# Kernel tuning notes

Measured on AMD Instinct MI355X. Metric: run time of the kernel, lower is better.

## Reference

```python
import jax, jax.numpy as jnp
import numpy as np

T, H, E, K = 256, 2048, 60, 4          # tokens, hidden, num_experts, top_k
F, FS = 1408, 5632                      # moe_intermediate, shared_expert_intermediate


def setup_inputs() -> dict:
    key = jax.random.key(0)
    ks = jax.random.split(key, 9)
    s = 0.02  # weight init scale to keep activations sane
    return {
        "hidden_states": jax.random.normal(ks[0], (T, H), jnp.float32),
        "gate_w": jax.random.normal(ks[1], (H, E), jnp.float32) * s,       # router
        "w_gate": jax.random.normal(ks[2], (E, H, F), jnp.float32) * s,    # expert gate proj
        "w_up": jax.random.normal(ks[3], (E, H, F), jnp.float32) * s,      # expert up proj
        "w_down": jax.random.normal(ks[4], (E, F, H), jnp.float32) * s,    # expert down proj
        "sw_gate": jax.random.normal(ks[5], (H, FS), jnp.float32) * s,     # shared expert gate proj
        "sw_up": jax.random.normal(ks[6], (H, FS), jnp.float32) * s,       # shared expert up proj
        "sw_down": jax.random.normal(ks[7], (FS, H), jnp.float32) * s,     # shared expert down proj
        "shared_gate_w": jax.random.normal(ks[8], (H, 1), jnp.float32) * s,  # shared expert sigmoid gate
    }


def reference(hidden_states, gate_w, w_gate, w_up, w_down, sw_gate, sw_up, sw_down, shared_gate_w):
    x = hidden_states                                  # [T, H]
    # --- router: softmax then top-k (DefaultMoeRoutingMethod, no renorm) ---
    probs = jax.nn.softmax(x @ gate_w, axis=-1)        # [T, E]
    vals, idx = jax.lax.top_k(probs, K)                # [T, K]
    tok = jnp.arange(x.shape[0])[:, None]
    comb = jnp.zeros_like(probs).at[tok, idx].set(vals)  # dense combine weights [T, E]
    # --- experts: gated SiLU MLP per expert, combine-weighted (down is linear,
    #     so scaling the pre-down activation by comb equals scaling the output) ---
    g = jnp.einsum('th,ehf->tef', x, w_gate)           # [T, E, F]
    u = jnp.einsum('th,ehf->tef', x, w_up)             # [T, E, F]
    a = (jax.nn.silu(g) * u) * comb[:, :, None]
    moe_out = jnp.einsum('tef,efh->th', a, w_down)     # [T, H]
    # --- shared expert with sigmoid gate ---
    sh = (jax.nn.silu(x @ sw_gate) * (x @ sw_up)) @ sw_down   # [T, H]
    sh = jax.nn.sigmoid(x @ shared_gate_w) * sh
    return moe_out + sh
```

## Files before the change

### kernel.cpp

```cpp
#include <hip/hip_runtime.h>
#include <hip/hip_bf16.h>
#include <stdint.h>

typedef unsigned short ushort_t;
typedef uint32_t u32;
typedef __attribute__((ext_vector_type(8))) __bf16 bf16x8;
typedef __attribute__((ext_vector_type(8))) unsigned short u16x8;
typedef __attribute__((ext_vector_type(4))) float f32x4;

#define T_  256
#define H_  2048
#define E_  60
#define F_  1408
#define FS_ 5632

__device__ __forceinline__ u32 rne2(float lo, float hi){
  u32 a = __builtin_bit_cast(u32, lo);
  u32 b = __builtin_bit_cast(u32, hi);
  a += 0x7FFFu + ((a >> 16) & 1u);
  b += 0x7FFFu + ((b >> 16) & 1u);
  return (a >> 16) | (b & 0xFFFF0000u);
}
__device__ __forceinline__ ushort_t rne1(float f){
  u32 a = __builtin_bit_cast(u32, f);
  a += 0x7FFFu + ((a >> 16) & 1u);
  return (ushort_t)(a >> 16);
}
__device__ __forceinline__ f32x4 zero4(){ f32x4 z; z[0]=0.f; z[1]=0.f; z[2]=0.f; z[3]=0.f; return z; }

__device__ __forceinline__ bf16x8 ldsbS(const float* p, const int S){
  union { u32 u[4]; bf16x8 v; } cv;
  cv.u[0] = rne2(p[0],   p[S]);
  cv.u[1] = rne2(p[2*S], p[3*S]);
  cv.u[2] = rne2(p[4*S], p[5*S]);
  cv.u[3] = rne2(p[6*S], p[7*S]);
  return cv.v;
}
__device__ __forceinline__ bf16x8 loada(const ushort_t* p){
  return __builtin_bit_cast(bf16x8, *(const u16x8*)p);
}
__device__ __forceinline__ void gload16(const float* g, float* l){
  __builtin_amdgcn_global_load_lds(
      (const __attribute__((address_space(1))) void*)g,
      (__attribute__((address_space(3))) void*)l, 16, 0, 0);
}
#define MFMA(a,b,c) __builtin_amdgcn_mfma_f32_16x16x32_bf16((a),(b),(c),0,0,0)

#define VMW(n)  asm volatile("s_waitcnt vmcnt(" #n ")" ::: "memory")
#define BARM()  asm volatile("s_barrier" ::: "memory")
#define SCH()   __builtin_amdgcn_sched_barrier(0)

__global__ __launch_bounds__(256) void k_router(
    const float* __restrict__ x, const float* __restrict__ gw,
    const float* __restrict__ sgw, ushort_t* __restrict__ xb,
    int* __restrict__ tk_idx, float* __restrict__ tk_val, float* __restrict__ sig)
{
  const int t = blockIdx.x, tid = threadIdx.x;
  const float* xr = x + (size_t)t * H_;
  {
    const float4 v0 = *(const float4*)(xr + tid*8);
    const float4 v1 = *(const float4*)(xr + tid*8 + 4);
    u32* dst = (u32*)(xb + (size_t)t*H_ + tid*8);
    dst[0] = rne2(v0.x, v0.y); dst[1] = rne2(v0.z, v0.w);
    dst[2] = rne2(v1.x, v1.y); dst[3] = rne2(v1.z, v1.w);
  }
  __shared__ float s_part[4][64];
  __shared__ float s_logit[64];
  __shared__ float s_red[256];
  const int e = tid & 63, q = tid >> 6;
  float p = 0.f;
  if (e < E_) {
    const float* g = gw + e;
    for (int h = q*512; h < q*512 + 512; ++h) p += xr[h] * g[h*E_];
  }
  s_part[q][e] = p;
  float sp = 0.f;
  for (int h = tid; h < H_; h += 256) sp += xr[h] * sgw[h];
  s_red[tid] = sp;
  __syncthreads();
  if (tid < 64) s_logit[tid] = s_part[0][tid] + s_part[1][tid] + s_part[2][tid] + s_part[3][tid];
  for (int s = 128; s > 0; s >>= 1) {
    if (tid < s) s_red[tid] += s_red[tid + s];
    __syncthreads();
  }
  if (tid == 0) {
    sig[t] = 1.f / (1.f + expf(-s_red[0]));
    float mx = -3.4e38f;
    for (int i = 0; i < E_; ++i) mx = fmaxf(mx, s_logit[i]);
    float sum = 0.f;
    for (int i = 0; i < E_; ++i) sum += expf(s_logit[i] - mx);
    for (int k = 0; k < 4; ++k) {
      float bv = -3.4e38f; int bi = 0;
      for (int i = 0; i < E_; ++i) { float v = s_logit[i]; if (v > bv) { bv = v; bi = i; } }
      tk_idx[t*4 + k] = bi;
      tk_val[t*4 + k] = expf(bv - mx) / sum;
      s_logit[bi] = -3.4e38f;
    }
  }
}

__global__ void k_lists(const int* __restrict__ tk_idx, const float* __restrict__ tk_val,
                        int* __restrict__ cnt, int* __restrict__ ltok,
                        int* __restrict__ lpair, float* __restrict__ lwt)
{
  const int e = threadIdx.x;
  if (e >= E_) return;
  int c = 0;
  for (int t = 0; t < T_; ++t) {
    #pragma unroll
    for (int k = 0; k < 4; ++k) {
      int ei = tk_idx[t*4 + k];
      if (ei == e && c < 64) {
        ltok[e*64 + c] = t;
        lpair[e*64 + c] = t*4 + k;
        lwt[e*64 + c] = tk_val[t*4 + k];
        ++c;
      }
    }
  }
  cnt[e] = c;
}

__global__ __launch_bounds__(256) void k_moe_gu(
    const ushort_t* __restrict__ xb, const float* __restrict__ wg_all,
    const float* __restrict__ wu_all, const int* __restrict__ cnt,
    const int* __restrict__ ltok, const float* __restrict__ lwt,
    ushort_t* __restrict__ act)
{
  __shared__ float lds[2][2*32*128];
  const int e = blockIdx.y;
  int m = cnt[e];
  if (m == 0) return;
  if (m > 64) m = 64;
  const int tid = threadIdx.x, wave = tid >> 6, lane = tid & 63;
  const int ln15 = lane & 15, kg = lane >> 4;
  const int col0 = blockIdx.x * 128;
  const size_t wbase = (size_t)e * ((size_t)H_ * F_) + col0;
  const float* gsg = wg_all + wbase + (size_t)(lane >> 5) * F_ + (lane & 31) * 4;
  const float* gsu = wu_all + wbase + (size_t)(lane >> 5) * F_ + (lane & 31) * 4;
  const int r0 = wave * 8;

  const ushort_t* ap[4];
  #pragma unroll
  for (int rt = 0; rt < 4; ++rt) {
    int row = rt*16 + ln15;
    int tok = ltok[e*64 + (row < m ? row : m-1)];
    ap[rt] = xb + (size_t)tok * H_ + kg*8;
  }

  f32x4 ag[4][2], au[4][2];
  #pragma unroll
  for (int i = 0; i < 4; ++i) { ag[i][0]=zero4(); ag[i][1]=zero4(); au[i][0]=zero4(); au[i][1]=zero4(); }
  bf16x8 a0[4], a1[4];

#define GU_STAGE(B, K0) do { \
    _Pragma("unroll") for (int i2 = 0; i2 < 4; ++i2) { \
      int r_ = r0 + i2*2; \
      gload16(gsg + (size_t)(K0 + r_) * F_, &lds[B][r_*128]); \
      gload16(gsu + (size_t)(K0 + r_) * F_, &lds[B][4096 + r_*128]); \
    } } while(0)
#define GU_ALOAD(D, K0) do { \
    _Pragma("unroll") for (int rt = 0; rt < 4; ++rt) D[rt] = loada(ap[rt] + (K0)); } while(0)
#define GU_COMPUTE(B, A) do { \
    const float* lg_ = &lds[B][kg*1024 + wave*32 + ln15]; \
    bf16x8 bg0_ = ldsbS(lg_, 128), bg1_ = ldsbS(lg_ + 16, 128); \
    bf16x8 bu0_ = ldsbS(lg_ + 4096, 128), bu1_ = ldsbS(lg_ + 4112, 128); \
    _Pragma("unroll") for (int rt = 0; rt < 4; ++rt) { \
      ag[rt][0] = MFMA(A[rt], bg0_, ag[rt][0]); \
      ag[rt][1] = MFMA(A[rt], bg1_, ag[rt][1]); \
      au[rt][0] = MFMA(A[rt], bu0_, au[rt][0]); \
      au[rt][1] = MFMA(A[rt], bu1_, au[rt][1]); \
    } } while(0)

  GU_ALOAD(a0, 0);  GU_STAGE(0, 0);
  GU_ALOAD(a1, 32); GU_STAGE(1, 32);
  for (int t = 0; t + 2 < 64; t += 2) {
    VMW(12); BARM(); SCH();
    GU_COMPUTE(0, a0);
    BARM();
    GU_ALOAD(a0, (t+2)*32); GU_STAGE(0, (t+2)*32);
    VMW(12); BARM(); SCH();
    GU_COMPUTE(1, a1);
    BARM();
    GU_ALOAD(a1, (t+3)*32); GU_STAGE(1, (t+3)*32);
  }
  VMW(12); BARM(); SCH();
  GU_COMPUTE(0, a0);
  VMW(0); BARM(); SCH();
  GU_COMPUTE(1, a1);

  #pragma unroll
  for (int rt = 0; rt < 4; ++rt)
    #pragma unroll
    for (int nt = 0; nt < 2; ++nt)
      #pragma unroll
      for (int j = 0; j < 4; ++j) {
        int r = rt*16 + kg*4 + j;
        if (r < m) {
          float wt = lwt[e*64 + r];
          float g = ag[rt][nt][j], u = au[rt][nt][j];
          float a = g / (1.f + __expf(-g)) * u * wt;
          act[((size_t)e*64 + r) * F_ + col0 + wave*32 + nt*16 + ln15] = rne1(a);
        }
      }
}

__global__ __launch_bounds__(256) void k_moe_down(
    const ushort_t* __restrict__ act, const float* __restrict__ wd_all,
    const int* __restrict__ cnt, const int* __restrict__ lpair,
    float* __restrict__ out4)
{
  __shared__ float lds[2][32*128];
  __shared__ int s_pair[64];
  const int e = blockIdx.y;
  int m = cnt[e];
  if (m == 0) return;
  if (m > 64) m = 64;
  const int tid = threadIdx.x, wave = tid >> 6, lane = tid & 63;
  const int ln15 = lane & 15, kg = lane >> 4;
  if (tid < 64) s_pair[tid] = (tid < m) ? lpair[e*64 + tid] : 0;
  const int col0 = blockIdx.x * 128;
  const float* gsd = wd_all + (size_t)e * ((size_t)F_ * H_) + col0
                   + (size_t)(lane >> 5) * H_ + (lane & 31) * 4;
  const int r0 = wave * 8;

  const ushort_t* ap[4];
  #pragma unroll
  for (int rt = 0; rt < 4; ++rt)
    ap[rt] = act + ((size_t)e*64 + rt*16 + ln15) * F_ + kg*8;

  f32x4 ac[4][2];
  #pragma unroll
  for (int i = 0; i < 4; ++i) { ac[i][0]=zero4(); ac[i][1]=zero4(); }
  bf16x8 a0[4], a1[4];

#define DN_STAGE(B, K0) do { \
    _Pragma("unroll") for (int i2 = 0; i2 < 4; ++i2) { \
      int r_ = r0 + i2*2; \
      gload16(gsd + (size_t)(K0 + r_) * H_, &lds[B][r_*128]); \
    } } while(0)
#define DN_ALOAD(D, K0) do { \
    _Pragma("unroll") for (int rt = 0; rt < 4; ++rt) D[rt] = loada(ap[rt] + (K0)); } while(0)
#define DN_COMPUTE(B, A) do { \
    const float* lw_ = &lds[B][kg*1024 + wave*32 + ln15]; \
    bf16x8 b0_ = ldsbS(lw_, 128), b1_ = ldsbS(lw_ + 16, 128); \
    _Pragma("unroll") for (int rt = 0; rt < 4; ++rt) { \
      ac[rt][0] = MFMA(A[rt], b0_, ac[rt][0]); \
      ac[rt][1] = MFMA(A[rt], b1_, ac[rt][1]); \
    } } while(0)

  DN_ALOAD(a0, 0);  DN_STAGE(0, 0);
  DN_ALOAD(a1, 32); DN_STAGE(1, 32);
  for (int t = 0; t + 2 < 44; t += 2) {
    VMW(8); BARM(); SCH();
    DN_COMPUTE(0, a0);
    BARM();
    DN_ALOAD(a0, (t+2)*32); DN_STAGE(0, (t+2)*32);
    VMW(8); BARM(); SCH();
    DN_COMPUTE(1, a1);
    BARM();
    DN_ALOAD(a1, (t+3)*32); DN_STAGE(1, (t+3)*32);
  }
  VMW(8); BARM(); SCH();
  DN_COMPUTE(0, a0);
  VMW(0); BARM(); SCH();
  DN_COMPUTE(1, a1);

  #pragma unroll
  for (int rt = 0; rt < 4; ++rt)
    #pragma unroll
    for (int nt = 0; nt < 2; ++nt)
      #pragma unroll
      for (int j = 0; j < 4; ++j) {
        int r = rt*16 + kg*4 + j;
        if (r < m)
          out4[(size_t)s_pair[r] * H_ + col0 + wave*32 + nt*16 + ln15] = ac[rt][nt][j];
      }
}

__global__ __launch_bounds__(256) void k_sh_gu(
    const ushort_t* __restrict__ xb, const float* __restrict__ swg,
    const float* __restrict__ swu, ushort_t* __restrict__ acts)
{
  __shared__ float lds[2][2048];
  const int tid = threadIdx.x, wave = tid >> 6, lane = tid & 63;
  const int ln15 = lane & 15, kg = lane >> 4;
  const int cb = blockIdx.x * 32;
  const int rowb = wave * 64;
  const int r0 = wave * 8;
  const float* gsg = swg + (size_t)(lane >> 3) * FS_ + cb + (lane & 7) * 4;
  const float* gsu = swu + (size_t)(lane >> 3) * FS_ + cb + (lane & 7) * 4;

  const ushort_t* ap[4];
  #pragma unroll
  for (int rt = 0; rt < 4; ++rt)
    ap[rt] = xb + (size_t)(rowb + rt*16 + ln15) * H_ + kg*8;

  f32x4 ag[4][2], au[4][2];
  #pragma unroll
  for (int i = 0; i < 4; ++i) { ag[i][0]=zero4(); ag[i][1]=zero4(); au[i][0]=zero4(); au[i][1]=zero4(); }
  bf16x8 a0[4], a1[4];

#define SG_STAGE(B, K0) do { \
    gload16(gsg + (size_t)(K0 + r0) * FS_, &lds[B][r0*32]); \
    gload16(gsu + (size_t)(K0 + r0) * FS_, &lds[B][1024 + r0*32]); \
  } while(0)
#define SG_ALOAD(D, K0) do { \
    _Pragma("unroll") for (int rt = 0; rt < 4; ++rt) D[rt] = loada(ap[rt] + (K0)); } while(0)
#define SG_COMPUTE(B, A) do { \
    const float* lg_ = &lds[B][kg*256 + ln15]; \
    bf16x8 bg0_ = ldsbS(lg_, 32), bg1_ = ldsbS(lg_ + 16, 32); \
    bf16x8 bu0_ = ldsbS(lg_ + 1024, 32), bu1_ = ldsbS(lg_ + 1040, 32); \
    _Pragma("unroll") for (int rt = 0; rt < 4; ++rt) { \
      ag[rt][0] = MFMA(A[rt], bg0_, ag[rt][0]); \
      ag[rt][1] = MFMA(A[rt], bg1_, ag[rt][1]); \
      au[rt][0] = MFMA(A[rt], bu0_, au[rt][0]); \
      au[rt][1] = MFMA(A[rt], bu1_, au[rt][1]); \
    } } while(0)

  SG_ALOAD(a0, 0);  SG_STAGE(0, 0);
  SG_ALOAD(a1, 32); SG_STAGE(1, 32);
  for (int t = 0; t + 2 < 64; t += 2) {
    VMW(6); BARM(); SCH();
    SG_COMPUTE(0, a0);
    BARM();
    SG_ALOAD(a0, (t+2)*32); SG_STAGE(0, (t+2)*32);
    VMW(6); BARM(); SCH();
    SG_COMPUTE(1, a1);
    BARM();
    SG_ALOAD(a1, (t+3)*32); SG_STAGE(1, (t+3)*32);
  }
  VMW(6); BARM(); SCH();
  SG_COMPUTE(0, a0);
  VMW(0); BARM(); SCH();
  SG_COMPUTE(1, a1);

  #pragma unroll
  for (int rt = 0; rt < 4; ++rt)
    #pragma unroll
    for (int nt = 0; nt < 2; ++nt)
      #pragma unroll
      for (int j = 0; j < 4; ++j) {
        int row = rowb + rt*16 + kg*4 + j;
        float g = ag[rt][nt][j], u = au[rt][nt][j];
        acts[(size_t)row * FS_ + cb + nt*16 + ln15] = rne1(g / (1.f + __expf(-g)) * u);
      }
}

__global__ __launch_bounds__(256) void k_sh_down(
    const ushort_t* __restrict__ acts, const float* __restrict__ swd,
    float* __restrict__ acc4)
{
  __shared__ float lds[2][2048];
  const int tid = threadIdx.x, wave = tid >> 6, lane = tid & 63;
  const int ln15 = lane & 15, kg = lane >> 4;
  const int cb = blockIdx.x * 64;
  const int kh = blockIdx.y;
  const int rowb = wave * 64;
  const int r0 = wave * 8;
  const float* gsd = swd + (size_t)(kh*1408) * H_ + cb
                   + (size_t)(lane >> 4) * H_ + (lane & 15) * 4;

  const ushort_t* ap[4];
  #pragma unroll
  for (int rt = 0; rt < 4; ++rt)
    ap[rt] = acts + (size_t)(rowb + rt*16 + ln15) * FS_ + kh*1408 + kg*8;

  f32x4 ac[4][4];
  #pragma unroll
  for (int i = 0; i < 4; ++i)
    #pragma unroll
    for (int c = 0; c < 4; ++c) ac[i][c] = zero4();
  bf16x8 a0[4], a1[4];

#define SD_STAGE(B, K0) do { \
    gload16(gsd + (size_t)(K0 + r0) * H_,     &lds[B][r0*64]); \
    gload16(gsd + (size_t)(K0 + r0 + 4) * H_, &lds[B][(r0+4)*64]); \
  } while(0)
#define SD_ALOAD(D, K0) do { \
    _Pragma("unroll") for (int rt = 0; rt < 4; ++rt) D[rt] = loada(ap[rt] + (K0)); } while(0)
#define SD_COMPUTE(B, A) do { \
    const float* lw_ = &lds[B][kg*512 + ln15]; \
    bf16x8 b0_ = ldsbS(lw_, 64),      b1_ = ldsbS(lw_ + 16, 64); \
    bf16x8 b2_ = ldsbS(lw_ + 32, 64), b3_ = ldsbS(lw_ + 48, 64); \
    _Pragma("unroll") for (int rt = 0; rt < 4; ++rt) { \
      ac[rt][0] = MFMA(A[rt], b0_, ac[rt][0]); \
      ac[rt][1] = MFMA(A[rt], b1_, ac[rt][1]); \
      ac[rt][2] = MFMA(A[rt], b2_, ac[rt][2]); \
      ac[rt][3] = MFMA(A[rt], b3_, ac[rt][3]); \
    } } while(0)

  SD_ALOAD(a0, 0);  SD_STAGE(0, 0);
  SD_ALOAD(a1, 32); SD_STAGE(1, 32);
  for (int t = 0; t + 2 < 44; t += 2) {
    VMW(6); BARM(); SCH();
    SD_COMPUTE(0, a0);
    BARM();
    SD_ALOAD(a0, (t+2)*32); SD_STAGE(0, (t+2)*32);
    VMW(6); BARM(); SCH();
    SD_COMPUTE(1, a1);
    BARM();
    SD_ALOAD(a1, (t+3)*32); SD_STAGE(1, (t+3)*32);
  }
  VMW(6); BARM(); SCH();
  SD_COMPUTE(0, a0);
  VMW(0); BARM(); SCH();
  SD_COMPUTE(1, a1);

  #pragma unroll
  for (int rt = 0; rt < 4; ++rt)
    #pragma unroll
    for (int c = 0; c < 4; ++c)
      #pragma unroll
      for (int j = 0; j < 4; ++j) {
        int row = rowb + rt*16 + kg*4 + j;
        acc4[((size_t)kh * T_ + row) * H_ + cb + c*16 + ln15] = ac[rt][c][j];
      }
}

__global__ __launch_bounds__(256) void k_final(
    const float* __restrict__ acc4, const float* __restrict__ out4,
    const float* __restrict__ sig, float* __restrict__ out)
{
  const int idx = blockIdx.x * blockDim.x + threadIdx.x;
  const int t = idx >> 9;
  const int h = (idx & 511) * 4;
  float ox = 0.f, oy = 0.f, oz = 0.f, ow = 0.f;
  #pragma unroll
  for (int s = 0; s < 4; ++s) {
    const float4 v = *(const float4*)(acc4 + ((size_t)s * T_ + t) * H_ + h);
    ox += v.x; oy += v.y; oz += v.z; ow += v.w;
  }
  const float sg = sig[t];
  ox *= sg; oy *= sg; oz *= sg; ow *= sg;
  #pragma unroll
  for (int k = 0; k < 4; ++k) {
    const float4 e4 = *(const float4*)(out4 + (size_t)(t*4 + k) * H_ + h);
    ox += e4.x; oy += e4.y; oz += e4.z; ow += e4.w;
  }
  float4 o; o.x = ox; o.y = oy; o.z = oz; o.w = ow;
  *(float4*)(out + (size_t)t * H_ + h) = o;
}

extern "C" void kernel_launch(void* const* d_in, const int* in_sizes, int n_in,
                              void* d_out, int out_size, void* d_ws, size_t ws_size,
                              hipStream_t stream)
{
  (void)in_sizes; (void)n_in; (void)out_size; (void)ws_size;
  const float* x   = (const float*)d_in[0];
  const float* gw  = (const float*)d_in[1];
  const float* wg  = (const float*)d_in[2];
  const float* wu  = (const float*)d_in[3];
  const float* wd  = (const float*)d_in[4];
  const float* swg = (const float*)d_in[5];
  const float* swu = (const float*)d_in[6];
  const float* swd = (const float*)d_in[7];
  const float* sgw = (const float*)d_in[8];

  char* ws = (char*)d_ws;
  ushort_t* xb    = (ushort_t*)(ws);
  ushort_t* act   = (ushort_t*)(ws + 1048576);
  ushort_t* acts  = (ushort_t*)(ws + 11862016);
  float*    out4  = (float*)   (ws + 14745600);
  float*    acc4  = (float*)   (ws + 23134208);
  float*    sig   = (float*)   (ws + 31522816);
  int*      tkidx = (int*)     (ws + 31523840);
  float*    tkval = (float*)   (ws + 31527936);
  int*      cnt   = (int*)     (ws + 31532032);
  int*      ltok  = (int*)     (ws + 31532288);
  int*      lpair = (int*)     (ws + 31547648);
  float*    lwt   = (float*)   (ws + 31563008);

  k_router  <<<T_, 256, 0, stream>>>(x, gw, sgw, xb, tkidx, tkval, sig);
  k_lists   <<<1, 64, 0, stream>>>(tkidx, tkval, cnt, ltok, lpair, lwt);
  k_moe_gu  <<<dim3(F_/128, E_), 256, 0, stream>>>(xb, wg, wu, cnt, ltok, lwt, act);
  k_moe_down<<<dim3(H_/128, E_), 256, 0, stream>>>(act, wd, cnt, lpair, out4);
  k_sh_gu   <<<dim3(FS_/32), 256, 0, stream>>>(xb, swg, swu, acts);
  k_sh_down <<<dim3(H_/64, 4), 256, 0, stream>>>(acts, swd, acc4);
  k_final   <<<512, 256, 0, stream>>>(acc4, out4, sig, (float*)d_out);
}
```

Baseline: 671.8 us.

## Halve MoE expert column tile to 64 and stage routing lists through LDS

The expert gate/up and down kernels now use 64-column tiles instead of 128, doubling the grid along the column axis. This gives more blocks for the weight-streaming, memory-bound expert GEMMs across the GPU's CUs, at the cost of more redundant activation loads and fewer MFMAs per LDS fetch. The list-building kernel also loads the top-k indices and values into shared memory with 256 threads before each expert scans them, replacing repeated global reads.

```diff
diff --git a/kernel.cpp b/kernel.cpp
--- a/kernel.cpp
+++ b/kernel.cpp
@@ -99,23 +99,25 @@
   }
 }
 
-__global__ void k_lists(const int* __restrict__ tk_idx, const float* __restrict__ tk_val,
-                        int* __restrict__ cnt, int* __restrict__ ltok,
-                        int* __restrict__ lpair, float* __restrict__ lwt)
-{
-  const int e = threadIdx.x;
+__global__ __launch_bounds__(256) void k_lists(
+    const int* __restrict__ tk_idx, const float* __restrict__ tk_val,
+    int* __restrict__ cnt, int* __restrict__ ltok,
+    int* __restrict__ lpair, float* __restrict__ lwt)
+{
+  __shared__ int   s_idx[1024];
+  __shared__ float s_val[1024];
+  const int tid = threadIdx.x;
+  for (int i = tid; i < 1024; i += 256) { s_idx[i] = tk_idx[i]; s_val[i] = tk_val[i]; }
+  __syncthreads();
+  const int e = tid;
   if (e >= E_) return;
   int c = 0;
-  for (int t = 0; t < T_; ++t) {
-    #pragma unroll
-    for (int k = 0; k < 4; ++k) {
-      int ei = tk_idx[t*4 + k];
-      if (ei == e && c < 64) {
-        ltok[e*64 + c] = t;
-        lpair[e*64 + c] = t*4 + k;
-        lwt[e*64 + c] = tk_val[t*4 + k];
-        ++c;
-      }
+  for (int i = 0; i < 1024; ++i) {
+    if (s_idx[i] == e && c < 64) {
+      ltok[e*64 + c]  = i >> 2;
+      lpair[e*64 + c] = i;
+      lwt[e*64 + c]   = s_val[i];
+      ++c;
     }
   }
   cnt[e] = c;
@@ -127,17 +129,17 @@
     const int* __restrict__ ltok, const float* __restrict__ lwt,
     ushort_t* __restrict__ act)
 {
-  __shared__ float lds[2][2*32*128];
+  __shared__ float lds[2][2*32*64];
   const int e = blockIdx.y;
   int m = cnt[e];
   if (m == 0) return;
   if (m > 64) m = 64;
   const int tid = threadIdx.x, wave = tid >> 6, lane = tid & 63;
   const int ln15 = lane & 15, kg = lane >> 4;
-  const int col0 = blockIdx.x * 128;
+  const int col0 = blockIdx.x * 64;
   const size_t wbase = (size_t)e * ((size_t)H_ * F_) + col0;
-  const float* gsg = wg_all + wbase + (size_t)(lane >> 5) * F_ + (lane & 31) * 4;
-  const float* gsu = wu_all + wbase + (size_t)(lane >> 5) * F_ + (lane & 31) * 4;
+  const float* gsg = wg_all + wbase + (size_t)(lane >> 4) * F_ + (lane & 15) * 4;
+  const float* gsu = wu_all + wbase + (size_t)(lane >> 4) * F_ + (lane & 15) * 4;
   const int r0 = wave * 8;
 
   const ushort_t* ap[4];
@@ -148,43 +150,41 @@
     ap[rt] = xb + (size_t)tok * H_ + kg*8;
   }
 
-  f32x4 ag[4][2], au[4][2];
-  #pragma unroll
-  for (int i = 0; i < 4; ++i) { ag[i][0]=zero4(); ag[i][1]=zero4(); au[i][0]=zero4(); au[i][1]=zero4(); }
+  f32x4 ag[4], au[4];
+  #pragma unroll
+  for (int i = 0; i < 4; ++i) { ag[i] = zero4(); au[i] = zero4(); }
   bf16x8 a0[4], a1[4];
 
 #define GU_STAGE(B, K0) do { \
-    _Pragma("unroll") for (int i2 = 0; i2 < 4; ++i2) { \
-      int r_ = r0 + i2*2; \
-      gload16(gsg + (size_t)(K0 + r_) * F_, &lds[B][r_*128]); \
-      gload16(gsu + (size_t)(K0 + r_) * F_, &lds[B][4096 + r_*128]); \
-    } } while(0)
+    gload16(gsg + (size_t)(K0 + r0)     * F_, &lds[B][r0*64]); \
+    gload16(gsg + (size_t)(K0 + r0 + 4) * F_, &lds[B][(r0+4)*64]); \
+    gload16(gsu + (size_t)(K0 + r0)     * F_, &lds[B][2048 + r0*64]); \
+    gload16(gsu + (size_t)(K0 + r0 + 4) * F_, &lds[B][2048 + (r0+4)*64]); \
+  } while(0)
 #define GU_ALOAD(D, K0) do { \
     _Pragma("unroll") for (int rt = 0; rt < 4; ++rt) D[rt] = loada(ap[rt] + (K0)); } while(0)
 #define GU_COMPUTE(B, A) do { \
-    const float* lg_ = &lds[B][kg*1024 + wave*32 + ln15]; \
-    bf16x8 bg0_ = ldsbS(lg_, 128), bg1_ = ldsbS(lg_ + 16, 128); \
-    bf16x8 bu0_ = ldsbS(lg_ + 4096, 128), bu1_ = ldsbS(lg_ + 4112, 128); \
+    const float* lg_ = &lds[B][kg*512 + wave*16 + ln15]; \
+    bf16x8 bg_ = ldsbS(lg_, 64); \
+    bf16x8 bu_ = ldsbS(lg_ + 2048, 64); \
     _Pragma("unroll") for (int rt = 0; rt < 4; ++rt) { \
-      ag[rt][0] = MFMA(A[rt], bg0_, ag[rt][0]); \
-      ag[rt][1] = MFMA(A[rt], bg1_, ag[rt][1]); \
-      au[rt][0] = MFMA(A[rt], bu0_, au[rt][0]); \
-      au[rt][1] = MFMA(A[rt], bu1_, au[rt][1]); \
+      ag[rt] = MFMA(A[rt], bg_, ag[rt]); \
+      au[rt] = MFMA(A[rt], bu_, au[rt]); \
     } } while(0)
 
   GU_ALOAD(a0, 0);  GU_STAGE(0, 0);
   GU_ALOAD(a1, 32); GU_STAGE(1, 32);
   for (int t = 0; t + 2 < 64; t += 2) {
-    VMW(12); BARM(); SCH();
+    VMW(8); BARM(); SCH();
     GU_COMPUTE(0, a0);
     BARM();
     GU_ALOAD(a0, (t+2)*32); GU_STAGE(0, (t+2)*32);
-    VMW(12); BARM(); SCH();
+    VMW(8); BARM(); SCH();
     GU_COMPUTE(1, a1);
     BARM();
     GU_ALOAD(a1, (t+3)*32); GU_STAGE(1, (t+3)*32);
   }
-  VMW(12); BARM(); SCH();
+  VMW(8); BARM(); SCH();
   GU_COMPUTE(0, a0);
   VMW(0); BARM(); SCH();
   GU_COMPUTE(1, a1);
@@ -192,17 +192,15 @@
   #pragma unroll
   for (int rt = 0; rt < 4; ++rt)
     #pragma unroll
-    for (int nt = 0; nt < 2; ++nt)
-      #pragma unroll
-      for (int j = 0; j < 4; ++j) {
-        int r = rt*16 + kg*4 + j;
-        if (r < m) {
-          float wt = lwt[e*64 + r];
-          float g = ag[rt][nt][j], u = au[rt][nt][j];
-          float a = g / (1.f + __expf(-g)) * u * wt;
-          act[((size_t)e*64 + r) * F_ + col0 + wave*32 + nt*16 + ln15] = rne1(a);
-        }
+    for (int j = 0; j < 4; ++j) {
+      int r = rt*16 + kg*4 + j;
+      if (r < m) {
+        float wt = lwt[e*64 + r];
+        float g = ag[rt][j], u = au[rt][j];
+        float a = g / (1.f + __expf(-g)) * u * wt;
+        act[((size_t)e*64 + r) * F_ + col0 + wave*16 + ln15] = rne1(a);
       }
+    }
 }
 
 __global__ __launch_bounds__(256) void k_moe_down(
@@ -210,7 +208,7 @@
     const int* __restrict__ cnt, const int* __restrict__ lpair,
     float* __restrict__ out4)
 {
-  __shared__ float lds[2][32*128];
+  __shared__ float lds[2][32*64];
   __shared__ int s_pair[64];
   const int e = blockIdx.y;
   int m = cnt[e];
@@ -219,9 +217,9 @@
   const int tid = threadIdx.x, wave = tid >> 6, lane = tid & 63;
   const int ln15 = lane & 15, kg = lane >> 4;
   if (tid < 64) s_pair[tid] = (tid < m) ? lpair[e*64 + tid] : 0;
-  const int col0 = blockIdx.x * 128;
+  const int col0 = blockIdx.x * 64;
   const float* gsd = wd_all + (size_t)e * ((size_t)F_ * H_) + col0
-                   + (size_t)(lane >> 5) * H_ + (lane & 31) * 4;
+                   + (size_t)(lane >> 4) * H_ + (lane & 15) * 4;
   const int r0 = wave * 8;
 
   const ushort_t* ap[4];
@@ -229,39 +227,37 @@
   for (int rt = 0; rt < 4; ++rt)
     ap[rt] = act + ((size_t)e*64 + rt*16 + ln15) * F_ + kg*8;
 
-  f32x4 ac[4][2];
-  #pragma unroll
-  for (int i = 0; i < 4; ++i) { ac[i][0]=zero4(); ac[i][1]=zero4(); }
+  f32x4 ac[4];
+  #pragma unroll
+  for (int i = 0; i < 4; ++i) ac[i] = zero4();
   bf16x8 a0[4], a1[4];
 
 #define DN_STAGE(B, K0) do { \
-    _Pragma("unroll") for (int i2 = 0; i2 < 4; ++i2) { \
-      int r_ = r0 + i2*2; \
-      gload16(gsd + (size_t)(K0 + r_) * H_, &lds[B][r_*128]); \
-    } } while(0)
+    gload16(gsd + (size_t)(K0 + r0)     * H_, &lds[B][r0*64]); \
+    gload16(gsd + (size_t)(K0 + r0 + 4) * H_, &lds[B][(r0+4)*64]); \
+  } while(0)
 #define DN_ALOAD(D, K0) do { \
     _Pragma("unroll") for (int rt = 0; rt < 4; ++rt) D[rt] = loada(ap[rt] + (K0)); } while(0)
 #define DN_COMPUTE(B, A) do { \
-    const float* lw_ = &lds[B][kg*1024 + wave*32 + ln15]; \
-    bf16x8 b0_ = ldsbS(lw_, 128), b1_ = ldsbS(lw_ + 16, 128); \
-    _Pragma("unroll") for (int rt = 0; rt < 4; ++rt) { \
-      ac[rt][0] = MFMA(A[rt], b0_, ac[rt][0]); \
-      ac[rt][1] = MFMA(A[rt], b1_, ac[rt][1]); \
-    } } while(0)
+    const float* lw_ = &lds[B][kg*512 + wave*16 + ln15]; \
+    bf16x8 b_ = ldsbS(lw_, 64); \
+    _Pragma("unroll") for (int rt = 0; rt < 4; ++rt) \
+      ac[rt] = MFMA(A[rt], b_, ac[rt]); \
+  } while(0)
 
   DN_ALOAD(a0, 0);  DN_STAGE(0, 0);
   DN_ALOAD(a1, 32); DN_STAGE(1, 32);
   for (int t = 0; t + 2 < 44; t += 2) {
-    VMW(8); BARM(); SCH();
+    VMW(6); BARM(); SCH();
     DN_COMPUTE(0, a0);
     BARM();
     DN_ALOAD(a0, (t+2)*32); DN_STAGE(0, (t+2)*32);
-    VMW(8); BARM(); SCH();
+    VMW(6); BARM(); SCH();
     DN_COMPUTE(1, a1);
     BARM();
     DN_ALOAD(a1, (t+3)*32); DN_STAGE(1, (t+3)*32);
   }
-  VMW(8); BARM(); SCH();
+  VMW(6); BARM(); SCH();
   DN_COMPUTE(0, a0);
   VMW(0); BARM(); SCH();
   DN_COMPUTE(1, a1);
@@ -269,13 +265,11 @@
   #pragma unroll
   for (int rt = 0; rt < 4; ++rt)
     #pragma unroll
-    for (int nt = 0; nt < 2; ++nt)
-      #pragma unroll
-      for (int j = 0; j < 4; ++j) {
-        int r = rt*16 + kg*4 + j;
-        if (r < m)
-          out4[(size_t)s_pair[r] * H_ + col0 + wave*32 + nt*16 + ln15] = ac[rt][nt][j];
-      }
+    for (int j = 0; j < 4; ++j) {
+      int r = rt*16 + kg*4 + j;
+      if (r < m)
+        out4[(size_t)s_pair[r] * H_ + col0 + wave*16 + ln15] = ac[rt][j];
+    }
 }
 
 __global__ __launch_bounds__(256) void k_sh_gu(
@@ -472,9 +466,9 @@
   float*    lwt   = (float*)   (ws + 31563008);
 
   k_router  <<<T_, 256, 0, stream>>>(x, gw, sgw, xb, tkidx, tkval, sig);
-  k_lists   <<<1, 64, 0, stream>>>(tkidx, tkval, cnt, ltok, lpair, lwt);
-  k_moe_gu  <<<dim3(F_/128, E_), 256, 0, stream>>>(xb, wg, wu, cnt, ltok, lwt, act);
-  k_moe_down<<<dim3(H_/128, E_), 256, 0, stream>>>(act, wd, cnt, lpair, out4);
+  k_lists   <<<1, 256, 0, stream>>>(tkidx, tkval, cnt, ltok, lpair, lwt);
+  k_moe_gu  <<<dim3(F_/64, E_), 256, 0, stream>>>(xb, wg, wu, cnt, ltok, lwt, act);
+  k_moe_down<<<dim3(H_/64, E_), 256, 0, stream>>>(act, wd, cnt, lpair, out4);
   k_sh_gu   <<<dim3(FS_/32), 256, 0, stream>>>(xb, swg, swu, acts);
   k_sh_down <<<dim3(H_/64, 4), 256, 0, stream>>>(acts, swd, acc4);
   k_final   <<<512, 256, 0, stream>>>(acc4, out4, sig, (float*)d_out);
```

Result: slower. 716.3 us (+6.6%).

## Merge routed and shared expert GEMMs into two combined launches; widen down-proj tiles

Applied to the files above, without the earlier changes.

Combines the routed-expert gate/up kernel with the shared-expert gate/up kernel in one launch, and the routed down with the shared down in a second launch, with blocks picking their role by block index. The goal is to fill the GPU with independent work at once and to cut the tail effects of launching separate kernels back to back. The routed down projection now uses 256-column tiles, so each block reuses the activation tile across more columns. The list-building kernel stages top-k data in LDS and uses a flat scan. Each merged kernel reserves a fixed 64KB of LDS, which may reduce how many blocks fit on a CU.

```diff
diff --git a/kernel.cpp b/kernel.cpp
--- a/kernel.cpp
+++ b/kernel.cpp
@@ -99,70 +99,79 @@
   }
 }
 
-__global__ void k_lists(const int* __restrict__ tk_idx, const float* __restrict__ tk_val,
-                        int* __restrict__ cnt, int* __restrict__ ltok,
-                        int* __restrict__ lpair, float* __restrict__ lwt)
-{
-  const int e = threadIdx.x;
+__global__ __launch_bounds__(256) void k_lists(
+    const int* __restrict__ tk_idx, const float* __restrict__ tk_val,
+    int* __restrict__ cnt, int* __restrict__ ltok,
+    int* __restrict__ lpair, float* __restrict__ lwt)
+{
+  __shared__ int   s_idx[1024];
+  __shared__ float s_val[1024];
+  const int tid = threadIdx.x;
+  for (int i = tid; i < 1024; i += 256) { s_idx[i] = tk_idx[i]; s_val[i] = tk_val[i]; }
+  __syncthreads();
+  const int e = tid;
   if (e >= E_) return;
   int c = 0;
-  for (int t = 0; t < T_; ++t) {
-    #pragma unroll
-    for (int k = 0; k < 4; ++k) {
-      int ei = tk_idx[t*4 + k];
-      if (ei == e && c < 64) {
-        ltok[e*64 + c] = t;
-        lpair[e*64 + c] = t*4 + k;
-        lwt[e*64 + c] = tk_val[t*4 + k];
-        ++c;
-      }
+  for (int i = 0; i < 1024; ++i) {
+    if (s_idx[i] == e && c < 64) {
+      ltok[e*64 + c]  = i >> 2;
+      lpair[e*64 + c] = i;
+      lwt[e*64 + c]   = s_val[i];
+      ++c;
     }
   }
   cnt[e] = c;
 }
 
-__global__ __launch_bounds__(256) void k_moe_gu(
-    const ushort_t* __restrict__ xb, const float* __restrict__ wg_all,
-    const float* __restrict__ wu_all, const int* __restrict__ cnt,
-    const int* __restrict__ ltok, const float* __restrict__ lwt,
-    ushort_t* __restrict__ act)
-{
-  __shared__ float lds[2][2*32*128];
-  const int e = blockIdx.y;
-  int m = cnt[e];
-  if (m == 0) return;
-  if (m > 64) m = 64;
+__global__ __launch_bounds__(256) void k_mega1(
+    const ushort_t* __restrict__ xb,
+    const float* __restrict__ wg_all, const float* __restrict__ wu_all,
+    const int* __restrict__ cnt, const int* __restrict__ ltok,
+    const float* __restrict__ lwt, ushort_t* __restrict__ act,
+    const float* __restrict__ swg, const float* __restrict__ swu,
+    ushort_t* __restrict__ acts)
+{
+  __shared__ char smem[65536];
+  float* lds = (float*)smem;
+  const int bid = blockIdx.x;
   const int tid = threadIdx.x, wave = tid >> 6, lane = tid & 63;
   const int ln15 = lane & 15, kg = lane >> 4;
-  const int col0 = blockIdx.x * 128;
-  const size_t wbase = (size_t)e * ((size_t)H_ * F_) + col0;
-  const float* gsg = wg_all + wbase + (size_t)(lane >> 5) * F_ + (lane & 31) * 4;
-  const float* gsu = wu_all + wbase + (size_t)(lane >> 5) * F_ + (lane & 31) * 4;
-  const int r0 = wave * 8;
-
-  const ushort_t* ap[4];
-  #pragma unroll
-  for (int rt = 0; rt < 4; ++rt) {
-    int row = rt*16 + ln15;
-    int tok = ltok[e*64 + (row < m ? row : m-1)];
-    ap[rt] = xb + (size_t)tok * H_ + kg*8;
-  }
-
-  f32x4 ag[4][2], au[4][2];
-  #pragma unroll
-  for (int i = 0; i < 4; ++i) { ag[i][0]=zero4(); ag[i][1]=zero4(); au[i][0]=zero4(); au[i][1]=zero4(); }
-  bf16x8 a0[4], a1[4];
+
+  if (bid < 660) {
+    const int e  = bid / 11;
+    const int cx = bid % 11;
+    int m = cnt[e];
+    if (m == 0) return;
+    if (m > 64) m = 64;
+    const int col0 = cx * 128;
+    const size_t wbase = (size_t)e * ((size_t)H_ * F_) + col0;
+    const float* gsg = wg_all + wbase + (size_t)(lane >> 5) * F_ + (lane & 31) * 4;
+    const float* gsu = wu_all + wbase + (size_t)(lane >> 5) * F_ + (lane & 31) * 4;
+    const int r0 = wave * 8;
+
+    const ushort_t* ap[4];
+    #pragma unroll
+    for (int rt = 0; rt < 4; ++rt) {
+      int row = rt*16 + ln15;
+      int tok = ltok[e*64 + (row < m ? row : m-1)];
+      ap[rt] = xb + (size_t)tok * H_ + kg*8;
+    }
+
+    f32x4 ag[4][2], au[4][2];
+    #pragma unroll
+    for (int i = 0; i < 4; ++i) { ag[i][0]=zero4(); ag[i][1]=zero4(); au[i][0]=zero4(); au[i][1]=zero4(); }
+    bf16x8 a0[4], a1[4];
 
 #define GU_STAGE(B, K0) do { \
     _Pragma("unroll") for (int i2 = 0; i2 < 4; ++i2) { \
       int r_ = r0 + i2*2; \
-      gload16(gsg + (size_t)(K0 + r_) * F_, &lds[B][r_*128]); \
-      gload16(gsu + (size_t)(K0 + r_) * F_, &lds[B][4096 + r_*128]); \
+      gload16(gsg + (size_t)(K0 + r_) * F_, lds + (B)*8192 + r_*128); \
+      gload16(gsu + (size_t)(K0 + r_) * F_, lds + (B)*8192 + 4096 + r_*128); \
     } } while(0)
 #define GU_ALOAD(D, K0) do { \
     _Pragma("unroll") for (int rt = 0; rt < 4; ++rt) D[rt] = loada(ap[rt] + (K0)); } while(0)
 #define GU_COMPUTE(B, A) do { \
-    const float* lg_ = &lds[B][kg*1024 + wave*32 + ln15]; \
+    const float* lg_ = lds + (B)*8192 + kg*1024 + wave*32 + ln15; \
     bf16x8 bg0_ = ldsbS(lg_, 128), bg1_ = ldsbS(lg_ + 16, 128); \
     bf16x8 bu0_ = ldsbS(lg_ + 4096, 128), bu1_ = ldsbS(lg_ + 4112, 128); \
     _Pragma("unroll") for (int rt = 0; rt < 4; ++rt) { \
@@ -172,143 +181,63 @@
       au[rt][1] = MFMA(A[rt], bu1_, au[rt][1]); \
     } } while(0)
 
-  GU_ALOAD(a0, 0);  GU_STAGE(0, 0);
-  GU_ALOAD(a1, 32); GU_STAGE(1, 32);
-  for (int t = 0; t + 2 < 64; t += 2) {
+    GU_ALOAD(a0, 0);  GU_STAGE(0, 0);
+    GU_ALOAD(a1, 32); GU_STAGE(1, 32);
+    for (int t = 0; t + 2 < 64; t += 2) {
+      VMW(12); BARM(); SCH();
+      GU_COMPUTE(0, a0);
+      BARM();
+      GU_ALOAD(a0, (t+2)*32); GU_STAGE(0, (t+2)*32);
+      VMW(12); BARM(); SCH();
+      GU_COMPUTE(1, a1);
+      BARM();
+      GU_ALOAD(a1, (t+3)*32); GU_STAGE(1, (t+3)*32);
+    }
     VMW(12); BARM(); SCH();
     GU_COMPUTE(0, a0);
-    BARM();
-    GU_ALOAD(a0, (t+2)*32); GU_STAGE(0, (t+2)*32);
-    VMW(12); BARM(); SCH();
+    VMW(0); BARM(); SCH();
     GU_COMPUTE(1, a1);
-    BARM();
-    GU_ALOAD(a1, (t+3)*32); GU_STAGE(1, (t+3)*32);
-  }
-  VMW(12); BARM(); SCH();
-  GU_COMPUTE(0, a0);
-  VMW(0); BARM(); SCH();
-  GU_COMPUTE(1, a1);
-
-  #pragma unroll
-  for (int rt = 0; rt < 4; ++rt)
-    #pragma unroll
-    for (int nt = 0; nt < 2; ++nt)
-      #pragma unroll
-      for (int j = 0; j < 4; ++j) {
-        int r = rt*16 + kg*4 + j;
-        if (r < m) {
-          float wt = lwt[e*64 + r];
-          float g = ag[rt][nt][j], u = au[rt][nt][j];
-          float a = g / (1.f + __expf(-g)) * u * wt;
-          act[((size_t)e*64 + r) * F_ + col0 + wave*32 + nt*16 + ln15] = rne1(a);
+
+    #pragma unroll
+    for (int rt = 0; rt < 4; ++rt)
+      #pragma unroll
+      for (int nt = 0; nt < 2; ++nt)
+        #pragma unroll
+        for (int j = 0; j < 4; ++j) {
+          int r = rt*16 + kg*4 + j;
+          if (r < m) {
+            float wt = lwt[e*64 + r];
+            float g = ag[rt][nt][j], u = au[rt][nt][j];
+            float a = g / (1.f + __expf(-g)) * u * wt;
+            act[((size_t)e*64 + r) * F_ + col0 + wave*32 + nt*16 + ln15] = rne1(a);
+          }
         }
-      }
-}
-
-__global__ __launch_bounds__(256) void k_moe_down(
-    const ushort_t* __restrict__ act, const float* __restrict__ wd_all,
-    const int* __restrict__ cnt, const int* __restrict__ lpair,
-    float* __restrict__ out4)
-{
-  __shared__ float lds[2][32*128];
-  __shared__ int s_pair[64];
-  const int e = blockIdx.y;
-  int m = cnt[e];
-  if (m == 0) return;
-  if (m > 64) m = 64;
-  const int tid = threadIdx.x, wave = tid >> 6, lane = tid & 63;
-  const int ln15 = lane & 15, kg = lane >> 4;
-  if (tid < 64) s_pair[tid] = (tid < m) ? lpair[e*64 + tid] : 0;
-  const int col0 = blockIdx.x * 128;
-  const float* gsd = wd_all + (size_t)e * ((size_t)F_ * H_) + col0
-                   + (size_t)(lane >> 5) * H_ + (lane & 31) * 4;
-  const int r0 = wave * 8;
-
-  const ushort_t* ap[4];
-  #pragma unroll
-  for (int rt = 0; rt < 4; ++rt)
-    ap[rt] = act + ((size_t)e*64 + rt*16 + ln15) * F_ + kg*8;
-
-  f32x4 ac[4][2];
-  #pragma unroll
-  for (int i = 0; i < 4; ++i) { ac[i][0]=zero4(); ac[i][1]=zero4(); }
-  bf16x8 a0[4], a1[4];
-
-#define DN_STAGE(B, K0) do { \
-    _Pragma("unroll") for (int i2 = 0; i2 < 4; ++i2) { \
-      int r_ = r0 + i2*2; \
-      gload16(gsd + (size_t)(K0 + r_) * H_, &lds[B][r_*128]); \
-    } } while(0)
-#define DN_ALOAD(D, K0) do { \
-    _Pragma("unroll") for (int rt = 0; rt < 4; ++rt) D[rt] = loada(ap[rt] + (K0)); } while(0)
-#define DN_COMPUTE(B, A) do { \
-    const float* lw_ = &lds[B][kg*1024 + wave*32 + ln15]; \
-    bf16x8 b0_ = ldsbS(lw_, 128), b1_ = ldsbS(lw_ + 16, 128); \
-    _Pragma("unroll") for (int rt = 0; rt < 4; ++rt) { \
-      ac[rt][0] = MFMA(A[rt], b0_, ac[rt][0]); \
-      ac[rt][1] = MFMA(A[rt], b1_, ac[rt][1]); \
-    } } while(0)
-
-  DN_ALOAD(a0, 0);  DN_STAGE(0, 0);
-  DN_ALOAD(a1, 32); DN_STAGE(1, 32);
-  for (int t = 0; t + 2 < 44; t += 2) {
-    VMW(8); BARM(); SCH();
-    DN_COMPUTE(0, a0);
-    BARM();
-    DN_ALOAD(a0, (t+2)*32); DN_STAGE(0, (t+2)*32);
-    VMW(8); BARM(); SCH();
-    DN_COMPUTE(1, a1);
-    BARM();
-    DN_ALOAD(a1, (t+3)*32); DN_STAGE(1, (t+3)*32);
-  }
-  VMW(8); BARM(); SCH();
-  DN_COMPUTE(0, a0);
-  VMW(0); BARM(); SCH();
-  DN_COMPUTE(1, a1);
-
-  #pragma unroll
-  for (int rt = 0; rt < 4; ++rt)
-    #pragma unroll
-    for (int nt = 0; nt < 2; ++nt)
-      #pragma unroll
-      for (int j = 0; j < 4; ++j) {
-        int r = rt*16 + kg*4 + j;
-        if (r < m)
-          out4[(size_t)s_pair[r] * H_ + col0 + wave*32 + nt*16 + ln15] = ac[rt][nt][j];
-      }
-}
-
-__global__ __launch_bounds__(256) void k_sh_gu(
-    const ushort_t* __restrict__ xb, const float* __restrict__ swg,
-    const float* __restrict__ swu, ushort_t* __restrict__ acts)
-{
-  __shared__ float lds[2][2048];
-  const int tid = threadIdx.x, wave = tid >> 6, lane = tid & 63;
-  const int ln15 = lane & 15, kg = lane >> 4;
-  const int cb = blockIdx.x * 32;
-  const int rowb = wave * 64;
-  const int r0 = wave * 8;
-  const float* gsg = swg + (size_t)(lane >> 3) * FS_ + cb + (lane & 7) * 4;
-  const float* gsu = swu + (size_t)(lane >> 3) * FS_ + cb + (lane & 7) * 4;
-
-  const ushort_t* ap[4];
-  #pragma unroll
-  for (int rt = 0; rt < 4; ++rt)
-    ap[rt] = xb + (size_t)(rowb + rt*16 + ln15) * H_ + kg*8;
-
-  f32x4 ag[4][2], au[4][2];
-  #pragma unroll
-  for (int i = 0; i < 4; ++i) { ag[i][0]=zero4(); ag[i][1]=zero4(); au[i][0]=zero4(); au[i][1]=zero4(); }
-  bf16x8 a0[4], a1[4];
+  } else {
+    const int sb = bid - 660;
+    const int cb = sb * 32;
+    const int rowb = wave * 64;
+    const int r0 = wave * 8;
+    const float* gsg = swg + (size_t)(lane >> 3) * FS_ + cb + (lane & 7) * 4;
+    const float* gsu = swu + (size_t)(lane >> 3) * FS_ + cb + (lane & 7) * 4;
+
+    const ushort_t* ap[4];
+    #pragma unroll
+    for (int rt = 0; rt < 4; ++rt)
+      ap[rt] = xb + (size_t)(rowb + rt*16 + ln15) * H_ + kg*8;
+
+    f32x4 ag[4][2], au[4][2];
+    #pragma unroll
+    for (int i = 0; i < 4; ++i) { ag[i][0]=zero4(); ag[i][1]=zero4(); au[i][0]=zero4(); au[i][1]=zero4(); }
+    bf16x8 a0[4], a1[4];
 
 #define SG_STAGE(B, K0) do { \
-    gload16(gsg + (size_t)(K0 + r0) * FS_, &lds[B][r0*32]); \
-    gload16(gsu + (size_t)(K0 + r0) * FS_, &lds[B][1024 + r0*32]); \
+    gload16(gsg + (size_t)(K0 + r0) * FS_, lds + (B)*2048 + r0*32); \
+    gload16(gsu + (size_t)(K0 + r0) * FS_, lds + (B)*2048 + 1024 + r0*32); \
   } while(0)
 #define SG_ALOAD(D, K0) do { \
     _Pragma("unroll") for (int rt = 0; rt < 4; ++rt) D[rt] = loada(ap[rt] + (K0)); } while(0)
 #define SG_COMPUTE(B, A) do { \
-    const float* lg_ = &lds[B][kg*256 + ln15]; \
+    const float* lg_ = lds + (B)*2048 + kg*256 + ln15; \
     bf16x8 bg0_ = ldsbS(lg_, 32), bg1_ = ldsbS(lg_ + 16, 32); \
     bf16x8 bu0_ = ldsbS(lg_ + 1024, 32), bu1_ = ldsbS(lg_ + 1040, 32); \
     _Pragma("unroll") for (int rt = 0; rt < 4; ++rt) { \
@@ -318,69 +247,148 @@
       au[rt][1] = MFMA(A[rt], bu1_, au[rt][1]); \
     } } while(0)
 
-  SG_ALOAD(a0, 0);  SG_STAGE(0, 0);
-  SG_ALOAD(a1, 32); SG_STAGE(1, 32);
-  for (int t = 0; t + 2 < 64; t += 2) {
+    SG_ALOAD(a0, 0);  SG_STAGE(0, 0);
+    SG_ALOAD(a1, 32); SG_STAGE(1, 32);
+    for (int t = 0; t + 2 < 64; t += 2) {
+      VMW(6); BARM(); SCH();
+      SG_COMPUTE(0, a0);
+      BARM();
+      SG_ALOAD(a0, (t+2)*32); SG_STAGE(0, (t+2)*32);
+      VMW(6); BARM(); SCH();
+      SG_COMPUTE(1, a1);
+      BARM();
+      SG_ALOAD(a1, (t+3)*32); SG_STAGE(1, (t+3)*32);
+    }
     VMW(6); BARM(); SCH();
     SG_COMPUTE(0, a0);
-    BARM();
-    SG_ALOAD(a0, (t+2)*32); SG_STAGE(0, (t+2)*32);
-    VMW(6); BARM(); SCH();
+    VMW(0); BARM(); SCH();
     SG_COMPUTE(1, a1);
-    BARM();
-    SG_ALOAD(a1, (t+3)*32); SG_STAGE(1, (t+3)*32);
-  }
-  VMW(6); BARM(); SCH();
-  SG_COMPUTE(0, a0);
-  VMW(0); BARM(); SCH();
-  SG_COMPUTE(1, a1);
-
-  #pragma unroll
-  for (int rt = 0; rt < 4; ++rt)
-    #pragma unroll
-    for (int nt = 0; nt < 2; ++nt)
-      #pragma unroll
-      for (int j = 0; j < 4; ++j) {
-        int row = rowb + rt*16 + kg*4 + j;
-        float g = ag[rt][nt][j], u = au[rt][nt][j];
-        acts[(size_t)row * FS_ + cb + nt*16 + ln15] = rne1(g / (1.f + __expf(-g)) * u);
-      }
-}
-
-__global__ __launch_bounds__(256) void k_sh_down(
+
+    #pragma unroll
+    for (int rt = 0; rt < 4; ++rt)
+      #pragma unroll
+      for (int nt = 0; nt < 2; ++nt)
+        #pragma unroll
+        for (int j = 0; j < 4; ++j) {
+          int row = rowb + rt*16 + kg*4 + j;
+          float g = ag[rt][nt][j], u = au[rt][nt][j];
+          acts[(size_t)row * FS_ + cb + nt*16 + ln15] = rne1(g / (1.f + __expf(-g)) * u);
+        }
+  }
+}
+
+__global__ __launch_bounds__(256) void k_mega2(
+    const ushort_t* __restrict__ act, const float* __restrict__ wd_all,
+    const int* __restrict__ cnt, const int* __restrict__ lpair,
+    float* __restrict__ out4,
     const ushort_t* __restrict__ acts, const float* __restrict__ swd,
     float* __restrict__ acc4)
 {
-  __shared__ float lds[2][2048];
+  __shared__ char smem[65536];
+  float* lds = (float*)smem;
+  const int bid = blockIdx.x;
   const int tid = threadIdx.x, wave = tid >> 6, lane = tid & 63;
   const int ln15 = lane & 15, kg = lane >> 4;
-  const int cb = blockIdx.x * 64;
-  const int kh = blockIdx.y;
-  const int rowb = wave * 64;
-  const int r0 = wave * 8;
-  const float* gsd = swd + (size_t)(kh*1408) * H_ + cb
-                   + (size_t)(lane >> 4) * H_ + (lane & 15) * 4;
-
-  const ushort_t* ap[4];
-  #pragma unroll
-  for (int rt = 0; rt < 4; ++rt)
-    ap[rt] = acts + (size_t)(rowb + rt*16 + ln15) * FS_ + kh*1408 + kg*8;
-
-  f32x4 ac[4][4];
-  #pragma unroll
-  for (int i = 0; i < 4; ++i)
-    #pragma unroll
-    for (int c = 0; c < 4; ++c) ac[i][c] = zero4();
-  bf16x8 a0[4], a1[4];
+
+  if (bid < 480) {
+    const int e  = bid / 8;
+    const int cx = bid % 8;
+    int m = cnt[e];
+    if (m == 0) return;
+    if (m > 64) m = 64;
+    __shared__ int s_pair[64];
+    if (tid < 64) s_pair[tid] = (tid < m) ? lpair[e*64 + tid] : 0;
+    const int col0 = cx * 256;
+    const float* gsd = wd_all + (size_t)e * ((size_t)F_ * H_) + col0 + lane * 4;
+    const int r0 = wave * 8;
+    const int c0 = wave * 64;
+
+    const ushort_t* ap[4];
+    #pragma unroll
+    for (int rt = 0; rt < 4; ++rt)
+      ap[rt] = act + ((size_t)e*64 + rt*16 + ln15) * F_ + kg*8;
+
+    f32x4 ac[4][4];
+    #pragma unroll
+    for (int i = 0; i < 4; ++i)
+      #pragma unroll
+      for (int c = 0; c < 4; ++c) ac[i][c] = zero4();
+    bf16x8 a0[4], a1[4];
+
+#define DN_STAGE(B, K0) do { \
+    _Pragma("unroll") for (int i2 = 0; i2 < 8; ++i2) { \
+      int r_ = r0 + i2; \
+      gload16(gsd + (size_t)(K0 + r_) * H_, lds + (B)*8192 + r_*256); \
+    } } while(0)
+#define DN_ALOAD(D, K0) do { \
+    _Pragma("unroll") for (int rt = 0; rt < 4; ++rt) D[rt] = loada(ap[rt] + (K0)); } while(0)
+#define DN_COMPUTE(B, A) do { \
+    const float* lw_ = lds + (B)*8192 + kg*2048 + c0 + ln15; \
+    bf16x8 b0_ = ldsbS(lw_, 256),      b1_ = ldsbS(lw_ + 16, 256); \
+    bf16x8 b2_ = ldsbS(lw_ + 32, 256), b3_ = ldsbS(lw_ + 48, 256); \
+    _Pragma("unroll") for (int rt = 0; rt < 4; ++rt) { \
+      ac[rt][0] = MFMA(A[rt], b0_, ac[rt][0]); \
+      ac[rt][1] = MFMA(A[rt], b1_, ac[rt][1]); \
+      ac[rt][2] = MFMA(A[rt], b2_, ac[rt][2]); \
+      ac[rt][3] = MFMA(A[rt], b3_, ac[rt][3]); \
+    } } while(0)
+
+    DN_ALOAD(a0, 0);  DN_STAGE(0, 0);
+    DN_ALOAD(a1, 32); DN_STAGE(1, 32);
+    for (int t = 0; t + 2 < 44; t += 2) {
+      VMW(12); BARM(); SCH();
+      DN_COMPUTE(0, a0);
+      BARM();
+      DN_ALOAD(a0, (t+2)*32); DN_STAGE(0, (t+2)*32);
+      VMW(12); BARM(); SCH();
+      DN_COMPUTE(1, a1);
+      BARM();
+      DN_ALOAD(a1, (t+3)*32); DN_STAGE(1, (t+3)*32);
+    }
+    VMW(12); BARM(); SCH();
+    DN_COMPUTE(0, a0);
+    VMW(0); BARM(); SCH();
+    DN_COMPUTE(1, a1);
+
+    #pragma unroll
+    for (int rt = 0; rt < 4; ++rt)
+      #pragma unroll
+      for (int c = 0; c < 4; ++c)
+        #pragma unroll
+        for (int j = 0; j < 4; ++j) {
+          int r = rt*16 + kg*4 + j;
+          if (r < m)
+            out4[(size_t)s_pair[r] * H_ + col0 + c0 + c*16 + ln15] = ac[rt][c][j];
+        }
+  } else {
+    const int sb = bid - 480;
+    const int cb = (sb & 31) * 64;
+    const int kh = sb >> 5;
+    const int rowb = wave * 64;
+    const int r0 = wave * 8;
+    const float* gsd = swd + (size_t)(kh*1408) * H_ + cb
+                     + (size_t)(lane >> 4) * H_ + (lane & 15) * 4;
+
+    const ushort_t* ap[4];
+    #pragma unroll
+    for (int rt = 0; rt < 4; ++rt)
+      ap[rt] = acts + (size_t)(rowb + rt*16 + ln15) * FS_ + kh*1408 + kg*8;
+
+    f32x4 ac[4][4];
+    #pragma unroll
+    for (int i = 0; i < 4; ++i)
+      #pragma unroll
+      for (int c = 0; c < 4; ++c) ac[i][c] = zero4();
+    bf16x8 a0[4], a1[4];
 
 #define SD_STAGE(B, K0) do { \
-    gload16(gsd + (size_t)(K0 + r0) * H_,     &lds[B][r0*64]); \
-    gload16(gsd + (size_t)(K0 + r0 + 4) * H_, &lds[B][(r0+4)*64]); \
+    gload16(gsd + (size_t)(K0 + r0) * H_,     lds + (B)*2048 + r0*64); \
+    gload16(gsd + (size_t)(K0 + r0 + 4) * H_, lds + (B)*2048 + (r0+4)*64); \
   } while(0)
 #define SD_ALOAD(D, K0) do { \
     _Pragma("unroll") for (int rt = 0; rt < 4; ++rt) D[rt] = loada(ap[rt] + (K0)); } while(0)
 #define SD_COMPUTE(B, A) do { \
-    const float* lw_ = &lds[B][kg*512 + ln15]; \
+    const float* lw_ = lds + (B)*2048 + kg*512 + ln15; \
     bf16x8 b0_ = ldsbS(lw_, 64),      b1_ = ldsbS(lw_ + 16, 64); \
     bf16x8 b2_ = ldsbS(lw_ + 32, 64), b3_ = ldsbS(lw_ + 48, 64); \
     _Pragma("unroll") for (int rt = 0; rt < 4; ++rt) { \
@@ -390,32 +398,33 @@
       ac[rt][3] = MFMA(A[rt], b3_, ac[rt][3]); \
     } } while(0)
 
-  SD_ALOAD(a0, 0);  SD_STAGE(0, 0);
-  SD_ALOAD(a1, 32); SD_STAGE(1, 32);
-  for (int t = 0; t + 2 < 44; t += 2) {
+    SD_ALOAD(a0, 0);  SD_STAGE(0, 0);
+    SD_ALOAD(a1, 32); SD_STAGE(1, 32);
+    for (int t = 0; t + 2 < 44; t += 2) {
+      VMW(6); BARM(); SCH();
+      SD_COMPUTE(0, a0);
+      BARM();
+      SD_ALOAD(a0, (t+2)*32); SD_STAGE(0, (t+2)*32);
+      VMW(6); BARM(); SCH();
+      SD_COMPUTE(1, a1);
+      BARM();
+      SD_ALOAD(a1, (t+3)*32); SD_STAGE(1, (t+3)*32);
+    }
     VMW(6); BARM(); SCH();
     SD_COMPUTE(0, a0);
-    BARM();
-    SD_ALOAD(a0, (t+2)*32); SD_STAGE(0, (t+2)*32);
-    VMW(6); BARM(); SCH();
+    VMW(0); BARM(); SCH();
     SD_COMPUTE(1, a1);
-    BARM();
-    SD_ALOAD(a1, (t+3)*32); SD_STAGE(1, (t+3)*32);
-  }
-  VMW(6); BARM(); SCH();
-  SD_COMPUTE(0, a0);
-  VMW(0); BARM(); SCH();
-  SD_COMPUTE(1, a1);
-
-  #pragma unroll
-  for (int rt = 0; rt < 4; ++rt)
-    #pragma unroll
-    for (int c = 0; c < 4; ++c)
-      #pragma unroll
-      for (int j = 0; j < 4; ++j) {
-        int row = rowb + rt*16 + kg*4 + j;
-        acc4[((size_t)kh * T_ + row) * H_ + cb + c*16 + ln15] = ac[rt][c][j];
-      }
+
+    #pragma unroll
+    for (int rt = 0; rt < 4; ++rt)
+      #pragma unroll
+      for (int c = 0; c < 4; ++c)
+        #pragma unroll
+        for (int j = 0; j < 4; ++j) {
+          int row = rowb + rt*16 + kg*4 + j;
+          acc4[((size_t)kh * T_ + row) * H_ + cb + c*16 + ln15] = ac[rt][c][j];
+        }
+  }
 }
 
 __global__ __launch_bounds__(256) void k_final(
@@ -471,11 +480,9 @@
   int*      lpair = (int*)     (ws + 31547648);
   float*    lwt   = (float*)   (ws + 31563008);
 
-  k_router  <<<T_, 256, 0, stream>>>(x, gw, sgw, xb, tkidx, tkval, sig);
-  k_lists   <<<1, 64, 0, stream>>>(tkidx, tkval, cnt, ltok, lpair, lwt);
-  k_moe_gu  <<<dim3(F_/128, E_), 256, 0, stream>>>(xb, wg, wu, cnt, ltok, lwt, act);
-  k_moe_down<<<dim3(H_/128, E_), 256, 0, stream>>>(act, wd, cnt, lpair, out4);
-  k_sh_gu   <<<dim3(FS_/32), 256, 0, stream>>>(xb, swg, swu, acts);
-  k_sh_down <<<dim3(H_/64, 4), 256, 0, stream>>>(acts, swd, acc4);
-  k_final   <<<512, 256, 0, stream>>>(acc4, out4, sig, (float*)d_out);
-}
+  k_router<<<T_, 256, 0, stream>>>(x, gw, sgw, xb, tkidx, tkval, sig);
+  k_lists <<<1, 256, 0, stream>>>(tkidx, tkval, cnt, ltok, lpair, lwt);
+  k_mega1 <<<660 + 176, 256, 0, stream>>>(xb, wg, wu, cnt, ltok, lwt, act, swg, swu, acts);
+  k_mega2 <<<480 + 128, 256, 0, stream>>>(act, wd, cnt, lpair, out4, acts, swd, acc4);
+  k_final <<<512, 256, 0, stream>>>(acc4, out4, sig, (float*)d_out);
+}
```

Measured after the change: 615.8 us (median of 2 runs). 8.3% less time.
